# Optimization experiments

Hardware: AMD Instinct MI355X
Metric: run time of the kernel (lower is better)

Reference implementation:

```python
import jax, jax.numpy as jnp
import numpy as np

N_NODES = 50000
N_EDGES = 800000
NODE_IN = 128
NODE_OUT = 64
EDGE_IN = 64
EDGE_OUT = 64
NEG_SLOPE = 0.01  # torch F.leaky_relu default


def setup_inputs() -> dict:
    key = jax.random.key(0)
    k = jax.random.split(key, 6)
    h = jax.random.normal(k[0], (N_NODES, NODE_IN), dtype=jnp.float32)
    e = jax.random.normal(k[1], (N_EDGES, EDGE_IN), dtype=jnp.float32)
    # Linear weights (bias=False), scaled roughly like torch default init
    Wn = jax.random.normal(k[2], (NODE_OUT, NODE_IN), dtype=jnp.float32) * (1.0 / np.sqrt(NODE_IN))
    We = jax.random.normal(k[3], (EDGE_OUT, EDGE_IN), dtype=jnp.float32) * (1.0 / np.sqrt(EDGE_IN))
    Wa = jax.random.normal(k[4], (1, EDGE_OUT + NODE_OUT), dtype=jnp.float32) * (1.0 / np.sqrt(EDGE_OUT + NODE_OUT))
    src = jax.random.randint(k[5], (N_EDGES,), 0, N_NODES, dtype=jnp.int32)
    return {"h": h, "e": e, "Wn": Wn, "We": We, "Wa": Wa, "src": src}


def reference(h, e, Wn, We, Wa, src):
    n_nodes = h.shape[0]
    node_feat = h @ Wn.T                         # [N, node_out] = fc_n(h)
    e_w = e @ We.T                               # [E, edge_out] = fc_e(e)
    src_ft = node_feat[src]                      # gather src node features per edge
    z2 = jnp.concatenate([e_w, src_ft], axis=-1) # [E, edge_out+node_out] (edge first, as in module)
    a = z2 @ Wa.T                                # [E, 1] attention logit
    e_lr = jnp.where(a >= 0, a, NEG_SLOPE * a)   # leaky_relu
    # segment softmax over edges grouped by src node (group_apply_edges softmax dim=1)
    m = jax.ops.segment_max(e_lr, src, num_segments=n_nodes)     # [N, 1]
    ex = jnp.exp(e_lr - m[src])
    denom = jax.ops.segment_sum(ex, src, num_segments=n_nodes)   # [N, 1]
    gamma = ex / denom[src]                      # [E, 1]
    e_weighted = gamma * e_w                     # [E, edge_out]
    return node_feat, e_weighted
```

## Files before the change

### kernel.cpp

```cpp
#include <hip/hip_runtime.h>


constexpr int kNodes   = 50000;
constexpr int kEdges   = 800000;
constexpr int kNodeIn  = 128;
constexpr int kNodeOut = 64;
constexpr int kEdgeIn  = 64;
constexpr int kEdgeOut = 64;
#define NEG_SLOPE 0.01f

typedef __attribute__((ext_vector_type(8))) short short8;
typedef __attribute__((ext_vector_type(4))) short short4v;
typedef __attribute__((ext_vector_type(4))) float f32x4;

constexpr int kOffV     = 0;
constexpr int kOffSn    = 64;
constexpr int kOffDenom = 50064;
constexpr int kOffEx    = 100064;
constexpr int kOffWeB   = 900064;
constexpr int kOffWnB   = 902112;
constexpr int kOffEbf   = 906240;

__device__ inline short f2bf(float x) {
    union { float f; unsigned u; } v; v.f = x;
    unsigned r = v.u + 0x7FFFu + ((v.u >> 16) & 1u);
    return (short)(r >> 16);
}

__global__ void k0_prep(const float* __restrict__ We, const float* __restrict__ Wn,
                        const float* __restrict__ Wa,
                        float* __restrict__ v, short* __restrict__ Web,
                        short* __restrict__ Wnb) {
    int t = threadIdx.x;
    if (t < kEdgeIn) {
        float acc = 0.f;
        #pragma unroll
        for (int c = 0; c < kEdgeOut; ++c) acc = fmaf(Wa[c], We[c * kEdgeIn + t], acc);
        v[t] = acc;
    }
    #pragma unroll
    for (int i = 0; i < (kEdgeOut * kEdgeIn) / 256; ++i)
        Web[i * 256 + t] = f2bf(We[i * 256 + t]);
    #pragma unroll
    for (int i = 0; i < (kNodeOut * kNodeIn) / 256; ++i)
        Wnb[i * 256 + t] = f2bf(Wn[i * 256 + t]);
}

__global__ __launch_bounds__(256) void k1_mfma(
    const float* __restrict__ h, const short* __restrict__ Wnb,
    const float* __restrict__ Wa, float* __restrict__ node_feat,
    float* __restrict__ s_n, float* __restrict__ denom) {
    const int lane = threadIdx.x & 63;
    const int l15  = lane & 15;
    const int lhi  = lane >> 4;
    const int n0   = blockIdx.x * 64 + (threadIdx.x >> 6) * 16;

    int gid = blockIdx.x * 256 + threadIdx.x;
    if (gid < kNodes) denom[gid] = 0.f;

    short8 Bf[4][4];
    #pragma unroll
    for (int kt = 0; kt < 4; ++kt)
        #pragma unroll
        for (int ct = 0; ct < 4; ++ct)
            Bf[kt][ct] = *reinterpret_cast<const short8*>(
                Wnb + (ct * 16 + l15) * kNodeIn + kt * 32 + lhi * 8);

    const int  arow   = n0 + l15;
    const bool avalid = arow < kNodes;
    const float* hrow = h + (size_t)arow * kNodeIn;

    f32x4 acc[4];
    #pragma unroll
    for (int ct = 0; ct < 4; ++ct) acc[ct] = (f32x4)(0.f);

    #pragma unroll
    for (int kt = 0; kt < 4; ++kt) {
        short8 af;
        if (avalid) {
            float4 t0 = *reinterpret_cast<const float4*>(hrow + kt * 32 + lhi * 8);
            float4 t1 = *reinterpret_cast<const float4*>(hrow + kt * 32 + lhi * 8 + 4);
            af[0] = f2bf(t0.x); af[1] = f2bf(t0.y); af[2] = f2bf(t0.z); af[3] = f2bf(t0.w);
            af[4] = f2bf(t1.x); af[5] = f2bf(t1.y); af[6] = f2bf(t1.z); af[7] = f2bf(t1.w);
        } else {
            #pragma unroll
            for (int j = 0; j < 8; ++j) af[j] = 0;
        }
        #pragma unroll
        for (int ct = 0; ct < 4; ++ct)
            acc[ct] = __builtin_amdgcn_mfma_f32_16x16x32_bf16(af, Bf[kt][ct], acc[ct], 0, 0, 0);
    }

    float wa[4];
    #pragma unroll
    for (int ct = 0; ct < 4; ++ct) wa[ct] = Wa[64 + ct * 16 + l15];

    #pragma unroll
    for (int reg = 0; reg < 4; ++reg) {
        int r = n0 + lhi * 4 + reg;
        bool rv = r < kNodes;
        float part = 0.f;
        #pragma unroll
        for (int ct = 0; ct < 4; ++ct) part = fmaf(wa[ct], acc[ct][reg], part);
        if (rv) {
            #pragma unroll
            for (int ct = 0; ct < 4; ++ct)
                __builtin_nontemporal_store(acc[ct][reg],
                    node_feat + (size_t)r * kNodeOut + ct * 16 + l15);
        }
        part += __shfl_xor(part, 1, 64);
        part += __shfl_xor(part, 2, 64);
        part += __shfl_xor(part, 4, 64);
        part += __shfl_xor(part, 8, 64);
        if (rv && l15 == 0) s_n[r] = part;
    }
}

__global__ __launch_bounds__(256) void kconv(
    const float* __restrict__ e, const float* __restrict__ v,
    short* __restrict__ ebf, float* __restrict__ av) {
    const int t   = threadIdx.x;
    const int q   = t & 15;
    const int rlo = t >> 4;
    const long base = (long)blockIdx.x * 64;

    float4 vv = reinterpret_cast<const float4*>(v)[q];

    #pragma unroll
    for (int it = 0; it < 4; ++it) {
        long r = base + it * 16 + rlo;
        float4 d = reinterpret_cast<const float4*>(e + r * kEdgeIn)[q];
        float part = d.x * vv.x + d.y * vv.y + d.z * vv.z + d.w * vv.w;
        part += __shfl_xor(part, 1, 64);
        part += __shfl_xor(part, 2, 64);
        part += __shfl_xor(part, 4, 64);
        part += __shfl_xor(part, 8, 64);
        short4v o;
        o[0] = f2bf(d.x); o[1] = f2bf(d.y); o[2] = f2bf(d.z); o[3] = f2bf(d.w);
        *reinterpret_cast<short4v*>(ebf + r * kEdgeIn + q * 4) = o;
        if (q == 0) av[r] = part;
    }
}

__global__ __launch_bounds__(256) void k2b(
    const int* __restrict__ src, const float* __restrict__ s_n,
    float* __restrict__ denom, float* __restrict__ ex) {
    int i = blockIdx.x * 256 + threadIdx.x;
    if (i >= kEdges) return;
    int s = src[i];
    float a = ex[i] + s_n[s];
    float lr = (a >= 0.f) ? a : NEG_SLOPE * a;
    float xe = __expf(lr);
    ex[i] = xe;
    atomicAdd(denom + s, xe);
}

__global__ __launch_bounds__(256) void k4_mfma(
    const short* __restrict__ ebf, const short* __restrict__ Web,
    const int* __restrict__ src, const float* __restrict__ denom,
    const float* __restrict__ ex, float* __restrict__ oute) {
    const int wave = threadIdx.x >> 6;
    const int lane = threadIdx.x & 63;
    const int l15  = lane & 15;
    const int lhi  = lane >> 4;
    const long base = (long)blockIdx.x * 256 + wave * 64;

    short8 Bf[2][4];
    #pragma unroll
    for (int kt = 0; kt < 2; ++kt)
        #pragma unroll
        for (int ct = 0; ct < 4; ++ct)
            Bf[kt][ct] = *reinterpret_cast<const short8*>(
                Web + (ct * 16 + l15) * kEdgeIn + kt * 32 + lhi * 8);

    f32x4 acc[4][4];
    #pragma unroll
    for (int m = 0; m < 4; ++m)
        #pragma unroll
        for (int n = 0; n < 4; ++n) acc[m][n] = (f32x4)(0.f);

    #pragma unroll
    for (int m = 0; m < 4; ++m) {
        const short* erow = ebf + (base + m * 16 + l15) * kEdgeIn;
        #pragma unroll
        for (int kt = 0; kt < 2; ++kt) {
            short8 af = *reinterpret_cast<const short8*>(erow + kt * 32 + lhi * 8);
            #pragma unroll
            for (int ct = 0; ct < 4; ++ct)
                acc[m][ct] = __builtin_amdgcn_mfma_f32_16x16x32_bf16(
                    af, Bf[kt][ct], acc[m][ct], 0, 0, 0);
        }
    }

    #pragma unroll
    for (int m = 0; m < 4; ++m) {
        const long r0 = base + m * 16 + lhi * 4;
        float4 exv = *reinterpret_cast<const float4*>(ex + r0);
        int4   sv  = *reinterpret_cast<const int4*>(src + r0);
        float ga[4];
        ga[0] = exv.x * __builtin_amdgcn_rcpf(denom[sv.x]);
        ga[1] = exv.y * __builtin_amdgcn_rcpf(denom[sv.y]);
        ga[2] = exv.z * __builtin_amdgcn_rcpf(denom[sv.z]);
        ga[3] = exv.w * __builtin_amdgcn_rcpf(denom[sv.w]);
        #pragma unroll
        for (int reg = 0; reg < 4; ++reg) {
            float gv = ga[reg];
            #pragma unroll
            for (int ct = 0; ct < 4; ++ct)
                __builtin_nontemporal_store(acc[m][ct][reg] * gv,
                    oute + (r0 + reg) * kEdgeOut + ct * 16 + l15);
        }
    }
}

extern "C" void kernel_launch(void* const* d_in, const int* in_sizes, int n_in,
                              void* d_out, int out_size, void* d_ws, size_t ws_size,
                              hipStream_t stream) {
    const float* h   = (const float*)d_in[0];
    const float* e   = (const float*)d_in[1];
    const float* Wn  = (const float*)d_in[2];
    const float* We  = (const float*)d_in[3];
    const float* Wa  = (const float*)d_in[4];
    const int*   src = (const int*)d_in[5];

    float* node_feat = (float*)d_out;
    float* oute      = (float*)d_out + (size_t)kNodes * kNodeOut;

    float* ws    = (float*)d_ws;
    float* v     = ws + kOffV;
    float* s_n   = ws + kOffSn;
    float* denom = ws + kOffDenom;
    float* ex    = ws + kOffEx;
    short* Web   = (short*)(ws + kOffWeB);
    short* Wnb   = (short*)(ws + kOffWnB);
    short* ebf   = (short*)(ws + kOffEbf);

    k0_prep<<<1, 256, 0, stream>>>(We, Wn, Wa, v, Web, Wnb);
    kconv<<<kEdges / 64, 256, 0, stream>>>(e, v, ebf, ex);
    k1_mfma<<<(kNodes + 63) / 64, 256, 0, stream>>>(h, Wnb, Wa, node_feat, s_n, denom);
    k2b<<<kEdges / 256, 256, 0, stream>>>(src, s_n, denom, ex);
    k4_mfma<<<kEdges / 256, 256, 0, stream>>>(ebf, Web, src, denom, ex, oute);
}
```

Before: 183.4 us.

## Fuse logit/exp/atomic pass into edge conversion kernel and parallelize weight prep

The separate edge-softmax kernel is removed. Its work (gather s_n, leaky relu, exp, atomic add into denom) now runs inside the edge conversion kernel, which is launched after the node GEMM so that s_n is ready. This avoids a launch and a round trip of the raw logits through memory. The weight-prep kernel is also spread over 48 blocks instead of one. In exchange, the node GEMM and the edge conversion are now serialized, and one lane in sixteen does the atomic work.

New measurement: 154.3 us. 1.19x faster.

```diff
diff --git a/kernel.cpp b/kernel.cpp
--- a/kernel.cpp
+++ b/kernel.cpp
@@ -31,19 +31,20 @@
                         const float* __restrict__ Wa,
                         float* __restrict__ v, short* __restrict__ Web,
                         short* __restrict__ Wnb) {
-    int t = threadIdx.x;
-    if (t < kEdgeIn) {
+    int b = blockIdx.x, t = threadIdx.x;
+    if (b == 0 && t < kEdgeIn) {
         float acc = 0.f;
         #pragma unroll
         for (int c = 0; c < kEdgeOut; ++c) acc = fmaf(Wa[c], We[c * kEdgeIn + t], acc);
         v[t] = acc;
     }
-    #pragma unroll
-    for (int i = 0; i < (kEdgeOut * kEdgeIn) / 256; ++i)
-        Web[i * 256 + t] = f2bf(We[i * 256 + t]);
-    #pragma unroll
-    for (int i = 0; i < (kNodeOut * kNodeIn) / 256; ++i)
-        Wnb[i * 256 + t] = f2bf(Wn[i * 256 + t]);
+    if (b < 16) {
+        int i = b * 256 + t;
+        Web[i] = f2bf(We[i]);
+    } else {
+        int i = (b - 16) * 256 + t;
+        Wnb[i] = f2bf(Wn[i]);
+    }
 }
 
 __global__ __launch_bounds__(256) void k1_mfma(
@@ -118,7 +119,9 @@
 
 __global__ __launch_bounds__(256) void kconv(
     const float* __restrict__ e, const float* __restrict__ v,
-    short* __restrict__ ebf, float* __restrict__ av) {
+    const int* __restrict__ src, const float* __restrict__ s_n,
+    float* __restrict__ denom, float* __restrict__ ex,
+    short* __restrict__ ebf) {
     const int t   = threadIdx.x;
     const int q   = t & 15;
     const int rlo = t >> 4;
@@ -138,21 +141,15 @@
         short4v o;
         o[0] = f2bf(d.x); o[1] = f2bf(d.y); o[2] = f2bf(d.z); o[3] = f2bf(d.w);
         *reinterpret_cast<short4v*>(ebf + r * kEdgeIn + q * 4) = o;
-        if (q == 0) av[r] = part;
-    }
-}
-
-__global__ __launch_bounds__(256) void k2b(
-    const int* __restrict__ src, const float* __restrict__ s_n,
-    float* __restrict__ denom, float* __restrict__ ex) {
-    int i = blockIdx.x * 256 + threadIdx.x;
-    if (i >= kEdges) return;
-    int s = src[i];
-    float a = ex[i] + s_n[s];
-    float lr = (a >= 0.f) ? a : NEG_SLOPE * a;
-    float xe = __expf(lr);
-    ex[i] = xe;
-    atomicAdd(denom + s, xe);
+        if (q == 0) {
+            int s = src[r];
+            float a = part + s_n[s];
+            float lr = (a >= 0.f) ? a : NEG_SLOPE * a;
+            float xe = __expf(lr);
+            ex[r] = xe;
+            atomicAdd(denom + s, xe);
+        }
+    }
 }
 
 __global__ __launch_bounds__(256) void k4_mfma(
@@ -235,9 +232,8 @@
     short* Wnb   = (short*)(ws + kOffWnB);
     short* ebf   = (short*)(ws + kOffEbf);
 
-    k0_prep<<<1, 256, 0, stream>>>(We, Wn, Wa, v, Web, Wnb);
-    kconv<<<kEdges / 64, 256, 0, stream>>>(e, v, ebf, ex);
+    k0_prep<<<48, 256, 0, stream>>>(We, Wn, Wa, v, Web, Wnb);
     k1_mfma<<<(kNodes + 63) / 64, 256, 0, stream>>>(h, Wnb, Wa, node_feat, s_n, denom);
-    k2b<<<kEdges / 256, 256, 0, stream>>>(src, s_n, denom, ex);
+    kconv<<<kEdges / 64, 256, 0, stream>>>(e, v, src, s_n, denom, ex, ebf);
     k4_mfma<<<kEdges / 256, 256, 0, stream>>>(ebf, Web, src, denom, ex, oute);
 }
```
